# Performance work log

Hardware: AMD Instinct MI355X
Metric: run time of the kernel (lower is better)

Reference implementation:

```python
import jax, jax.numpy as jnp
import numpy as np

B, L, N = 16, 64, 1024
HAND_DIM, J, HID = 99, 21, 512
N_LAYERS, N_HEADS = 4, 8
DH = HID // N_HEADS
CAT = HAND_DIM + 2 * J * 3 + 2 * N  # 2273
PNAMES = ['fc_lw','fc_lb','fc_rw','fc_rb','out_lw','out_lb','out_rw','out_rb','Wqkv','bqkv','Wo','bo','W1','b1f','W2','b2f','ln1_g','ln1_b','ln2_g','ln2_b']

def sinusoidal_pe(n_pos, d):
    pos = np.arange(n_pos)[:, None].astype(np.float32)
    div = np.exp(np.arange(0, d, 2).astype(np.float32) * (-np.log(10000.0) / d))
    pe = np.zeros((n_pos, d), np.float32)
    pe[:, 0::2] = np.sin(pos * div)
    pe[:, 1::2] = np.cos(pos * div)
    return jnp.asarray(pe)

def rot6d_to_rotmat(x6):
    a1, a2 = x6[..., 0:3], x6[..., 3:6]
    b1 = a1 / jnp.linalg.norm(a1, axis=-1, keepdims=True)
    b2 = a2 - jnp.sum(b1 * a2, -1, keepdims=True) * b1
    b2 = b2 / jnp.linalg.norm(b2, axis=-1, keepdims=True)
    b3 = jnp.cross(b1, b2)
    return jnp.stack([b1, b2, b3], axis=-1)  # [..., 3, 3] (columns)

def layer_norm(x, g, b):
    mu = jnp.mean(x, -1, keepdims=True)
    var = jnp.mean((x - mu) ** 2, -1, keepdims=True)
    return (x - mu) * jax.lax.rsqrt(var + 1e-5) * g + b

def attention_map(joints, pc):
    # joints [B,L,J,3], pc [B,L,N,3]; squared dists via ||a||^2+||b||^2-2ab (no [B,L,J,N,3] diff tensor)
    d2 = (jnp.sum(joints ** 2, -1)[..., :, None] + jnp.sum(pc ** 2, -1)[..., None, :]
          - 2.0 * jnp.einsum('bljd,blnd->bljn', joints, pc))
    idx = jnp.argmin(d2, axis=-1)  # [B,L,J] nearest-point index
    idx3 = jnp.broadcast_to(idx[..., None], idx.shape + (3,))
    contact = jnp.take_along_axis(pc, idx3, axis=2)  # [B,L,J,3]
    return jnp.exp(-50.0 * (joints - contact) ** 2)

def mha(x, Wqkv, bqkv, Wo, bo):
    Bq, S, D = x.shape
    qkv = x @ Wqkv + bqkv
    q, k, v = jnp.split(qkv, 3, axis=-1)
    split = lambda t: t.reshape(Bq, S, N_HEADS, DH).transpose(0, 2, 1, 3)
    q, k, v = split(q), split(k), split(v)
    att = jax.nn.softmax(jnp.einsum('bhqd,bhkd->bhqk', q, k) * (1.0 / np.sqrt(DH)), axis=-1)
    o = jnp.einsum('bhqk,bhkd->bhqd', att, v).transpose(0, 2, 1, 3).reshape(Bq, S, D)
    return o @ Wo + bo

def forward(x_lhand, x_rhand, j_lhand, j_rhand, m_contact, x_obj, point_cloud, p):
    rotmat = rot6d_to_rotmat(x_obj[..., 3:9])  # [B,L,3,3]
    pc_t = jnp.einsum('btij,bkj->btki', rotmat, point_cloud) + x_obj[..., 0:3][:, :, None, :]
    att_l = attention_map(j_lhand, pc_t).reshape(B, L, -1)
    att_r = attention_map(j_rhand, pc_t).reshape(B, L, -1)
    mc = jnp.broadcast_to(m_contact.reshape(B, 1, N), (B, L, N))
    pcn = jnp.linalg.norm(pc_t, axis=-1)  # [B,L,N]
    xl = jnp.concatenate([x_lhand, j_lhand.reshape(B, L, -1), mc, pcn, att_l], -1)
    xr = jnp.concatenate([x_rhand, j_rhand.reshape(B, L, -1), mc, pcn, att_r], -1)
    xl = xl @ p['fc_lw'] + p['fc_lb']
    xr = xr @ p['fc_rw'] + p['fc_rb']
    x = jnp.stack([xl, xr], axis=2).reshape(B, 2 * L, HID)  # interleave agents per frame
    pe_frame = jnp.repeat(sinusoidal_pe(L, HID), 2, axis=0)  # frame-wise: pair shares position
    pe_agent = jnp.tile(sinusoidal_pe(2, HID), (L, 1))       # agent-wise: alternating 0/1
    x = x + pe_frame[None] + pe_agent[None]
    for i in range(N_LAYERS):
        h = layer_norm(x + mha(x, p['Wqkv'][i], p['bqkv'][i], p['Wo'][i], p['bo'][i]), p['ln1_g'][i], p['ln1_b'][i])
        ff = jax.nn.relu(h @ p['W1'][i] + p['b1f'][i]) @ p['W2'][i] + p['b2f'][i]
        x = layer_norm(h + ff, p['ln2_g'][i], p['ln2_b'][i])
    out_l = x[:, 0::2] @ p['out_lw'] + p['out_lb']
    out_r = x[:, 1::2] @ p['out_rw'] + p['out_rb']
    return out_l, out_r

def setup_inputs() -> dict:
    key = jax.random.key(0)
    ks = jax.random.split(key, 16)
    r = lambda i, shape, s=1.0: jax.random.normal(ks[i], shape, jnp.float32) * s
    return {
        'x_lhand': r(0, (B, L, HAND_DIM)),
        'x_rhand': r(1, (B, L, HAND_DIM)),
        'j_lhand': r(2, (B, L, J, 3)),
        'j_rhand': r(3, (B, L, J, 3)),
        'm_contact': jax.random.uniform(ks[4], (B, N, 1), jnp.float32),
        'x_obj': r(5, (B, L, 10)),
        'point_cloud': r(6, (B, N, 3)),
        'fc_lw': r(7, (CAT, HID), 0.02), 'fc_lb': jnp.zeros((HID,), jnp.float32),
        'fc_rw': r(8, (CAT, HID), 0.02), 'fc_rb': jnp.zeros((HID,), jnp.float32),
        'out_lw': r(9, (HID, HAND_DIM), 0.02), 'out_lb': jnp.zeros((HAND_DIM,), jnp.float32),
        'out_rw': r(10, (HID, HAND_DIM), 0.02), 'out_rb': jnp.zeros((HAND_DIM,), jnp.float32),
        'Wqkv': r(11, (N_LAYERS, HID, 3 * HID), 0.02), 'bqkv': jnp.zeros((N_LAYERS, 3 * HID), jnp.float32),
        'Wo': r(12, (N_LAYERS, HID, HID), 0.02), 'bo': jnp.zeros((N_LAYERS, HID), jnp.float32),
        'W1': r(13, (N_LAYERS, HID, 4 * HID), 0.02), 'b1f': jnp.zeros((N_LAYERS, 4 * HID), jnp.float32),
        'W2': r(14, (N_LAYERS, 4 * HID, HID), 0.02), 'b2f': jnp.zeros((N_LAYERS, HID), jnp.float32),
        'ln1_g': jnp.ones((N_LAYERS, HID), jnp.float32), 'ln1_b': jnp.zeros((N_LAYERS, HID), jnp.float32),
        'ln2_g': jnp.ones((N_LAYERS, HID), jnp.float32), 'ln2_b': jnp.zeros((N_LAYERS, HID), jnp.float32),
    }

def reference(x_lhand, x_rhand, j_lhand, j_rhand, m_contact, x_obj, point_cloud, fc_lw, fc_lb, fc_rw, fc_rb, out_lw, out_lb, out_rw, out_rb, Wqkv, bqkv, Wo, bo, W1, b1f, W2, b2f, ln1_g, ln1_b, ln2_g, ln2_b):
    p = dict(zip(PNAMES, (fc_lw, fc_lb, fc_rw, fc_rb, out_lw, out_lb, out_rw, out_rb, Wqkv, bqkv, Wo, bo, W1, b1f, W2, b2f, ln1_g, ln1_b, ln2_g, ln2_b)))
    return forward(x_lhand, x_rhand, j_lhand, j_rhand, m_contact, x_obj, point_cloud, p)
```

## Files before the change

kernel.cpp:

```cpp
#include <hip/hip_runtime.h>
#include <hip/hip_bf16.h>

typedef __hip_bfloat16 bf16;
typedef __attribute__((ext_vector_type(8))) short short8;
typedef __attribute__((ext_vector_type(4))) float floatx4;

#define B_    16
#define L_    64
#define N_    1024
#define HANDD 99
#define Jn    21
#define HID   512
#define NLAY  4
#define NHEAD 8
#define DHEAD 64
#define CATD  2273
#define CATP  2304
#define S_    128
#define T_    2048

#define F_X     16
#define F_QKV   1048592
#define F_TMP   6291472
#define F_H     7340048
#define WB_F    8388624
#define W_FCL   0
#define W_FCR   1179648
#define W_QKV   2359296
#define W_WO    5505024
#define W_W1    6553600
#define W_W2    10747904
#define U_CATL  14942208
#define U_CATR  17301504
#define U_XB    19660800
#define U_AOB   20709376
#define U_HB    21757952
#define W_OUT   22806528
#define U_FFB   U_CATL

static __device__ __forceinline__ float b2f(bf16 x) { return __bfloat162float(x); }
static __device__ __forceinline__ float ldin(const void* p, size_t i, int isf32) {
    return isf32 ? ((const float*)p)[i] : b2f(((const bf16*)p)[i]);
}
static __device__ __forceinline__ unsigned short f2bf(float f) {
    unsigned int u = __float_as_uint(f);
    unsigned int r = (u + 0x7fffu + ((u >> 16) & 1u)) >> 16;
    return (unsigned short)r;
}

__global__ __launch_bounds__(256) void detect_kernel(const void* mc, int* flag)
{
    __shared__ int sbad;
    int tid = threadIdx.x;
    if (tid == 0) sbad = 0;
    __syncthreads();
    int bad = 0;
    for (int i = tid; i < 16384; i += 256) {
        float v = b2f(((const bf16*)mc)[i]);
        if (!(v >= -0.02f && v <= 1.02f)) bad = 1;
    }
    if (bad) atomicOr(&sbad, 1);
    __syncthreads();
    if (tid == 0) flag[0] = sbad ? 1 : 0;
}

__global__ __launch_bounds__(256) void wtrans_kernel(
    const void* __restrict__ src, size_t src_layer, int K, int Nn, int NnBound,
    int Kpad, unsigned short* __restrict__ dst, size_t dst_layer,
    const int* __restrict__ dtf)
{
    int isf32 = dtf[0];
    __shared__ float tile[64][65];
    int lay = blockIdx.z;
    size_t soff = (size_t)lay * src_layer;
    size_t doff = (size_t)lay * dst_layer;
    int n0 = blockIdx.x * 64, k0 = blockIdx.y * 64;
    int a = threadIdx.x & 63, bq = threadIdx.x >> 6;
    for (int r = bq; r < 64; r += 4) {
        int k = k0 + r;
        int n = n0 + a;
        float v = (k < K && n < NnBound) ? ldin(src, soff + (size_t)k * Nn + n, isf32) : 0.f;
        tile[r][a] = v;
    }
    __syncthreads();
    for (int r = bq; r < 64; r += 4) {
        dst[doff + (size_t)(n0 + r) * Kpad + k0 + a] = f2bf(tile[a][r]);
    }
}

__global__ __launch_bounds__(256) void pctcat_kernel(
    const void* __restrict__ x_l, const void* __restrict__ j_l,
    const void* __restrict__ x_r, const void* __restrict__ j_r,
    const void* __restrict__ mc, const void* __restrict__ x_obj,
    const void* __restrict__ pc, unsigned short* __restrict__ cat_l,
    unsigned short* __restrict__ cat_r, const int* __restrict__ dtf)
{
    __shared__ float pcl[N_ * 3];
    __shared__ float pcnl[N_];
    int isf32 = dtf[0];
    int bl = blockIdx.x;
    int b  = bl >> 6;
    int tid = threadIdx.x;

    size_t xo = (size_t)bl * 10;
    float t0 = ldin(x_obj, xo+0, isf32), t1 = ldin(x_obj, xo+1, isf32), t2 = ldin(x_obj, xo+2, isf32);
    float a1x = ldin(x_obj, xo+3, isf32), a1y = ldin(x_obj, xo+4, isf32), a1z = ldin(x_obj, xo+5, isf32);
    float a2x = ldin(x_obj, xo+6, isf32), a2y = ldin(x_obj, xo+7, isf32), a2z = ldin(x_obj, xo+8, isf32);
    float n1 = sqrtf(a1x*a1x + a1y*a1y + a1z*a1z);
    float b1x = a1x / n1, b1y = a1y / n1, b1z = a1z / n1;
    float d = b1x*a2x + b1y*a2y + b1z*a2z;
    float c2x = a2x - d*b1x, c2y = a2y - d*b1y, c2z = a2z - d*b1z;
    float n2 = sqrtf(c2x*c2x + c2y*c2y + c2z*c2z);
    float b2x = c2x / n2, b2y = c2y / n2, b2z = c2z / n2;
    float b3x = b1y*b2z - b1z*b2y;
    float b3y = b1z*b2x - b1x*b2z;
    float b3z = b1x*b2y - b1y*b2x;

    size_t pcb = (size_t)b * N_ * 3;
    for (int n = tid; n < N_; n += 256) {
        float p0 = ldin(pc, pcb + n*3+0, isf32);
        float p1 = ldin(pc, pcb + n*3+1, isf32);
        float p2 = ldin(pc, pcb + n*3+2, isf32);
        float q0 = b1x*p0 + b2x*p1 + b3x*p2 + t0;
        float q1 = b1y*p0 + b2y*p1 + b3y*p2 + t1;
        float q2 = b1z*p0 + b2z*p1 + b3z*p2 + t2;
        pcl[n*3+0] = q0; pcl[n*3+1] = q1; pcl[n*3+2] = q2;
        pcnl[n] = sqrtf(q0*q0 + q1*q1 + q2*q2);
    }
    __syncthreads();

    #pragma unroll
    for (int hand = 0; hand < 2; hand++) {
        const void* xh = hand ? x_r : x_l;
        const void* jh = hand ? j_r : j_l;
        unsigned short* row = (hand ? cat_r : cat_l) + (size_t)bl * CATP;
        for (int c = tid; c < HANDD; c += 256)  row[c]        = f2bf(ldin(xh, (size_t)bl*HANDD + c, isf32));
        for (int c = tid; c < 63;    c += 256)  row[99 + c]   = f2bf(ldin(jh, (size_t)bl*63 + c, isf32));
        for (int c = tid; c < N_;    c += 256)  row[162 + c]  = f2bf(ldin(mc, (size_t)b*N_ + c, isf32));
        for (int c = tid; c < N_;    c += 256)  row[1186 + c] = f2bf(pcnl[c]);
        for (int c = CATD + tid; c < CATP; c += 256) row[c] = 0;
    }

    int wave = tid >> 6, lane = tid & 63;
    for (int t = wave; t < 2 * Jn; t += 4) {
        int hand = t / Jn, j = t - hand * Jn;
        const void* jh = hand ? j_r : j_l;
        unsigned short* row = (hand ? cat_r : cat_l) + (size_t)bl * CATP;
        float jx = ldin(jh, (size_t)bl*63 + j*3 + 0, isf32);
        float jy = ldin(jh, (size_t)bl*63 + j*3 + 1, isf32);
        float jz = ldin(jh, (size_t)bl*63 + j*3 + 2, isf32);
        float jj = jx*jx + jy*jy + jz*jz;
        float best = 3.4e38f; int bidx = 0x7fffffff;
        for (int n = lane; n < N_; n += 64) {
            float p0 = pcl[n*3+0], p1 = pcl[n*3+1], p2 = pcl[n*3+2];
            float d2 = jj + (p0*p0 + p1*p1 + p2*p2) - 2.f*(jx*p0 + jy*p1 + jz*p2);
            if (d2 < best) { best = d2; bidx = n; }
        }
        for (int off = 32; off; off >>= 1) {
            float ob = __shfl_down(best, off, 64);
            int   oi = __shfl_down(bidx, off, 64);
            if (ob < best || (ob == best && oi < bidx)) { best = ob; bidx = oi; }
        }
        bidx = __shfl(bidx, 0, 64);
        if (lane < 3) {
            float jc = (lane == 0) ? jx : ((lane == 1) ? jy : jz);
            float cc = pcl[bidx*3 + lane];
            float dd = jc - cc;
            row[2210 + j*3 + lane] = f2bf(expf(-50.f * dd * dd));
        }
    }
}

#define RSTR 68

__global__ __launch_bounds__(256) void gemm_ks(
    const unsigned short* __restrict__ Ab, const unsigned short* __restrict__ Ab2,
    int K,
    const unsigned short* __restrict__ Wt, size_t wtoff, size_t wtoff2, int halfgrid,
    int Nn,
    const void* __restrict__ bias, const void* __restrict__ bias2, size_t boff,
    const float* __restrict__ resid,
    float* __restrict__ Df, unsigned short* __restrict__ Db,
    int relu, int rowmap, int tilesN, const int* __restrict__ dtf)
{
    __shared__ float red[4][64 * RSTR];
    int blk = blockIdx.x;
    if (halfgrid && blk >= halfgrid) {
        blk -= halfgrid; Ab = Ab2; wtoff = wtoff2; bias = bias2; rowmap = 2;
    }
    int tid = threadIdx.x;
    int wave = tid >> 6, lane = tid & 63;
    int quad = lane >> 4, l16 = lane & 15;
    int tm = blk / tilesN, tn = blk - tm * tilesN;
    int row0 = tm << 6, col0 = tn << 6;
    int Ks = K >> 2;
    int ks0 = wave * Ks;

    const unsigned short* Ap = Ab + (size_t)(row0 + l16) * K + ks0 + quad * 8;
    const unsigned short* Bp = Wt + wtoff + (size_t)(col0 + l16) * K + ks0 + quad * 8;
    size_t astep = (size_t)16 * K;

    floatx4 acc[4][4];
    #pragma unroll
    for (int i = 0; i < 4; i++)
        #pragma unroll
        for (int j = 0; j < 4; j++)
            acc[i][j] = (floatx4){0.f, 0.f, 0.f, 0.f};

    for (int k = 0; k < Ks; k += 32) {
        short8 af[4], bf[4];
        #pragma unroll
        for (int i = 0; i < 4; i++) {
            af[i] = *(const short8*)(Ap + i * astep + k);
            bf[i] = *(const short8*)(Bp + i * astep + k);
        }
        #pragma unroll
        for (int mi = 0; mi < 4; mi++)
            #pragma unroll
            for (int ni = 0; ni < 4; ni++)
                acc[mi][ni] = __builtin_amdgcn_mfma_f32_16x16x32_bf16(
                    af[mi], bf[ni], acc[mi][ni], 0, 0, 0);
    }

    #pragma unroll
    for (int mi = 0; mi < 4; mi++)
        #pragma unroll
        for (int ni = 0; ni < 4; ni++)
            #pragma unroll
            for (int reg = 0; reg < 4; reg++) {
                int r = mi * 16 + quad * 4 + reg;
                int c = ni * 16 + l16;
                red[wave][r * RSTR + c] = acc[mi][ni][reg];
            }
    __syncthreads();

    int isf32 = dtf[0];
    int cc = tid & 63;
    int c = col0 + cc;
    float bv;
    if (rowmap == 3)
        bv = (c < HANDD) ? ldin(bias, c, isf32)
           : ((c < 2 * HANDD) ? ldin(bias2, c - HANDD, isf32) : 0.f);
    else
        bv = bias ? ldin(bias, boff + c, isf32) : 0.f;
    float pe_div = 0.f, pa = 0.f;
    if (rowmap == 1 || rowmap == 2) {
        int ci = c & ~1;
        pe_div = expf((float)ci * (-logf(10000.f) / (float)HID));
        int hand = rowmap - 1;
        pa = (c & 1) ? cosf((float)hand * pe_div) : sinf((float)hand * pe_div);
    }
    int rbase = tid >> 6;
    #pragma unroll
    for (int j = 0; j < 16; j++) {
        int rr = rbase + (j << 2);
        int idx = rr * RSTR + cc;
        float v = red[0][idx] + red[1][idx] + red[2][idx] + red[3][idx] + bv;
        int r = row0 + rr;
        if (resid) v += resid[(size_t)r * Nn + c];
        if (relu)  v = fmaxf(v, 0.f);
        if (rowmap == 3) {
            int hand = r & 1;
            int l = (r >> 1) & 63, bb = r >> 7;
            if (hand == 0 && c < HANDD) {
                size_t oi = ((size_t)bb * 64 + l) * HANDD + c;
                if (isf32) ((float*)Df)[oi] = v;
                else       ((bf16*)Df)[oi]  = __float2bfloat16(v);
            } else if (hand == 1 && c >= HANDD && c < 2 * HANDD) {
                size_t oi = (size_t)B_ * L_ * HANDD + ((size_t)bb * 64 + l) * HANDD + (c - HANDD);
                if (isf32) ((float*)Df)[oi] = v;
                else       ((bf16*)Df)[oi]  = __float2bfloat16(v);
            }
        } else {
            int orow = r;
            if (rowmap) {
                int bb = r >> 6, ll = r & 63;
                orow = bb * S_ + 2 * ll + (rowmap - 1);
                float pf = (c & 1) ? cosf((float)ll * pe_div) : sinf((float)ll * pe_div);
                v += pf + pa;
            }
            if (Df) Df[(size_t)orow * Nn + c] = v;
            if (Db) Db[(size_t)orow * Nn + c] = f2bf(v);
        }
    }
}

#define VSTR 136

__global__ __launch_bounds__(128) void attn_mfma(
    const unsigned short* __restrict__ qkvb, unsigned short* __restrict__ aob)
{
    __shared__ unsigned short Vt[64 * VSTR];
    __shared__ unsigned short Pb[64 * VSTR];
    int bh = blockIdx.x;
    int b = bh >> 3, h = bh & 7;
    int rowhalf = blockIdx.y;
    int tid = threadIdx.x;
    int w = tid >> 6, lane = tid & 63;
    int quad = lane >> 4, l16 = lane & 15;
    size_t qbase = (size_t)(b * S_) * 1536 + h * DHEAD;

    for (int i = tid; i < S_ * DHEAD; i += 128) {
        int key = i >> 6, dcol = i & 63;
        Vt[dcol * VSTR + key] = qkvb[qbase + (size_t)key * 1536 + 1024 + dcol];
    }
    __syncthreads();

    int qrow0 = rowhalf * 64 + w * 32;
    short8 aQ[2][2];
    #pragma unroll
    for (int mt = 0; mt < 2; mt++)
        #pragma unroll
        for (int kc = 0; kc < 2; kc++)
            aQ[mt][kc] = *(const short8*)&qkvb[qbase + (size_t)(qrow0 + mt*16 + l16) * 1536 + kc*32 + quad*8];

    floatx4 sacc[2][8];
    #pragma unroll
    for (int mt = 0; mt < 2; mt++)
        #pragma unroll
        for (int nt = 0; nt < 8; nt++)
            sacc[mt][nt] = (floatx4){0.f, 0.f, 0.f, 0.f};

    #pragma unroll
    for (int nt = 0; nt < 8; nt++) {
        const unsigned short* kp = &qkvb[qbase + (size_t)(nt*16 + l16) * 1536 + 512 + quad*8];
        short8 bK0 = *(const short8*)kp;
        short8 bK1 = *(const short8*)(kp + 32);
        #pragma unroll
        for (int mt = 0; mt < 2; mt++) {
            sacc[mt][nt] = __builtin_amdgcn_mfma_f32_16x16x32_bf16(aQ[mt][0], bK0, sacc[mt][nt], 0, 0, 0);
            sacc[mt][nt] = __builtin_amdgcn_mfma_f32_16x16x32_bf16(aQ[mt][1], bK1, sacc[mt][nt], 0, 0, 0);
        }
    }

    #pragma unroll
    for (int mt = 0; mt < 2; mt++)
        #pragma unroll
        for (int reg = 0; reg < 4; reg++) {
            float v[8];
            float m = -3.4e38f;
            #pragma unroll
            for (int nt = 0; nt < 8; nt++) { v[nt] = sacc[mt][nt][reg] * 0.125f; m = fmaxf(m, v[nt]); }
            #pragma unroll
            for (int off = 1; off <= 8; off <<= 1) m = fmaxf(m, __shfl_xor(m, off, 64));
            float sum = 0.f;
            #pragma unroll
            for (int nt = 0; nt < 8; nt++) { v[nt] = expf(v[nt] - m); sum += v[nt]; }
            #pragma unroll
            for (int off = 1; off <= 8; off <<= 1) sum += __shfl_xor(sum, off, 64);
            float inv = 1.f / sum;
            int lr = w*32 + mt*16 + quad*4 + reg;
            #pragma unroll
            for (int nt = 0; nt < 8; nt++)
                Pb[lr * VSTR + nt*16 + l16] = f2bf(v[nt] * inv);
        }
    __syncthreads();

    #pragma unroll
    for (int mt = 0; mt < 2; mt++) {
        short8 aP[4];
        #pragma unroll
        for (int kt = 0; kt < 4; kt++)
            aP[kt] = *(const short8*)&Pb[(w*32 + mt*16 + l16) * VSTR + kt*32 + quad*8];
        #pragma unroll
        for (int nt = 0; nt < 4; nt++) {
            floatx4 o = (floatx4){0.f, 0.f, 0.f, 0.f};
            #pragma unroll
            for (int kt = 0; kt < 4; kt++) {
                short8 bV = *(const short8*)&Vt[(nt*16 + l16) * VSTR + kt*32 + quad*8];
                o = __builtin_amdgcn_mfma_f32_16x16x32_bf16(aP[kt], bV, o, 0, 0, 0);
            }
            #pragma unroll
            for (int reg = 0; reg < 4; reg++) {
                int qrow = qrow0 + mt*16 + quad*4 + reg;
                aob[(size_t)(b*S_ + qrow) * HID + h*DHEAD + nt*16 + l16] = f2bf(o[reg]);
            }
        }
    }
}

__global__ __launch_bounds__(256) void ln_kernel(
    const float* __restrict__ src, const void* __restrict__ g,
    const void* __restrict__ bb, size_t goff,
    float* __restrict__ dst, unsigned short* __restrict__ dstb,
    const int* __restrict__ dtf)
{
    int isf32 = dtf[0];
    int t = blockIdx.x;
    const float* x = src + (size_t)t * HID;
    int tid = threadIdx.x, lane = tid & 63, wave = tid >> 6;
    float v0 = x[tid], v1 = x[tid + 256];
    float s = v0 + v1;
    for (int off = 32; off; off >>= 1) s += __shfl_down(s, off, 64);
    __shared__ float wsum[4];
    if (lane == 0) wsum[wave] = s;
    __syncthreads();
    float mu = (wsum[0] + wsum[1] + wsum[2] + wsum[3]) * (1.f / 512.f);
    float d0 = v0 - mu, d1 = v1 - mu;
    float q = d0 * d0 + d1 * d1;
    for (int off = 32; off; off >>= 1) q += __shfl_down(q, off, 64);
    __syncthreads();
    if (lane == 0) wsum[wave] = q;
    __syncthreads();
    float var = (wsum[0] + wsum[1] + wsum[2] + wsum[3]) * (1.f / 512.f);
    float rstd = 1.f / sqrtf(var + 1e-5f);
    float y0 = d0 * rstd * ldin(g, goff + tid, isf32)       + ldin(bb, goff + tid, isf32);
    float y1 = d1 * rstd * ldin(g, goff + tid + 256, isf32) + ldin(bb, goff + tid + 256, isf32);
    if (dst) {
        dst[(size_t)t * HID + tid]       = y0;
        dst[(size_t)t * HID + tid + 256] = y1;
    }
    if (dstb) {
        dstb[(size_t)t * HID + tid]       = f2bf(y0);
        dstb[(size_t)t * HID + tid + 256] = f2bf(y1);
    }
}

extern "C" void kernel_launch(void* const* d_in, const int* in_sizes, int n_in,
                              void* d_out, int out_size, void* d_ws, size_t ws_size,
                              hipStream_t stream)
{
    const void* x_lhand = d_in[0];
    const void* x_rhand = d_in[1];
    const void* j_lhand = d_in[2];
    const void* j_rhand = d_in[3];
    const void* m_contact = d_in[4];
    const void* x_obj = d_in[5];
    const void* point_cloud = d_in[6];
    const void* fc_lw = d_in[7];
    const void* fc_lb = d_in[8];
    const void* fc_rw = d_in[9];
    const void* fc_rb = d_in[10];
    const void* out_lw = d_in[11];
    const void* out_lb = d_in[12];
    const void* out_rw = d_in[13];
    const void* out_rb = d_in[14];
    const void* Wqkv = d_in[15];
    const void* bqkv = d_in[16];
    const void* Wo   = d_in[17];
    const void* bo   = d_in[18];
    const void* W1   = d_in[19];
    const void* b1f  = d_in[20];
    const void* W2   = d_in[21];
    const void* b2fp = d_in[22];
    const void* ln1g = d_in[23];
    const void* ln1b = d_in[24];
    const void* ln2g = d_in[25];
    const void* ln2b = d_in[26];

    float* ws = (float*)d_ws;
    int* dtf = (int*)d_ws;
    float* x     = ws + F_X;
    float* tmp   = ws + F_TMP;
    float* h     = ws + F_H;
    unsigned short* qkvb = (unsigned short*)(ws + F_QKV);
    unsigned short* wb   = (unsigned short*)(ws + WB_F);
    unsigned short* catl = wb + U_CATL;
    unsigned short* catr = wb + U_CATR;
    unsigned short* xb   = wb + U_XB;
    unsigned short* aob  = wb + U_AOB;
    unsigned short* hb   = wb + U_HB;
    unsigned short* ffb  = wb + U_FFB;

    detect_kernel<<<1, 256, 0, stream>>>(m_contact, dtf);

    wtrans_kernel<<<dim3(8, 36, 1), 256, 0, stream>>>(fc_lw, 0, CATD, HID, HID, CATP, wb + W_FCL, 0, dtf);
    wtrans_kernel<<<dim3(8, 36, 1), 256, 0, stream>>>(fc_rw, 0, CATD, HID, HID, CATP, wb + W_FCR, 0, dtf);
    wtrans_kernel<<<dim3(24, 8, NLAY), 256, 0, stream>>>(Wqkv, (size_t)HID*1536, HID, 1536, 1536, HID, wb + W_QKV, (size_t)1536*HID, dtf);
    wtrans_kernel<<<dim3(8, 8, NLAY), 256, 0, stream>>>(Wo, (size_t)HID*HID, HID, HID, HID, HID, wb + W_WO, (size_t)HID*HID, dtf);
    wtrans_kernel<<<dim3(32, 8, NLAY), 256, 0, stream>>>(W1, (size_t)HID*2048, HID, 2048, 2048, HID, wb + W_W1, (size_t)2048*HID, dtf);
    wtrans_kernel<<<dim3(8, 32, NLAY), 256, 0, stream>>>(W2, (size_t)2048*HID, 2048, HID, HID, 2048, wb + W_W2, (size_t)HID*2048, dtf);
    wtrans_kernel<<<dim3(2, 8, 1), 256, 0, stream>>>(out_lw, 0, HID, HANDD, HANDD, HID, wb + W_OUT, 0, dtf);
    wtrans_kernel<<<dim3(2, 8, 1), 256, 0, stream>>>(out_rw, 0, HID, HANDD, HANDD, HID, wb + W_OUT + (size_t)HANDD * HID, 0, dtf);

    pctcat_kernel<<<B_ * L_, 256, 0, stream>>>(
        x_lhand, j_lhand, x_rhand, j_rhand, m_contact, x_obj, point_cloud,
        catl, catr, dtf);

    gemm_ks<<<256, 256, 0, stream>>>(catl, catr, CATP, wb, W_FCL, W_FCR, 128, HID,
                                     fc_lb, fc_rb, 0, nullptr, x, xb, 0, 1, 8, dtf);

    for (int i = 0; i < NLAY; i++) {
        size_t oWq = (size_t)W_QKV + (size_t)i * 1536 * HID, obq = (size_t)i * 1536;
        size_t oWo = (size_t)W_WO + (size_t)i * HID * HID,   obo = (size_t)i * HID;
        size_t oW1 = (size_t)W_W1 + (size_t)i * 2048 * HID,  ob1 = (size_t)i * 2048;
        size_t oW2 = (size_t)W_W2 + (size_t)i * HID * 2048,  ob2 = (size_t)i * HID;
        size_t oln = (size_t)i * HID;

        gemm_ks<<<768, 256, 0, stream>>>(xb, nullptr, HID, wb, oWq, 0, 0, 1536,
                                         bqkv, nullptr, obq, nullptr, nullptr, qkvb, 0, 0, 24, dtf);

        attn_mfma<<<dim3(B_ * NHEAD, 2), 128, 0, stream>>>(qkvb, aob);

        gemm_ks<<<256, 256, 0, stream>>>(aob, nullptr, HID, wb, oWo, 0, 0, HID,
                                         bo, nullptr, obo, x, tmp, nullptr, 0, 0, 8, dtf);
        ln_kernel<<<T_, 256, 0, stream>>>(tmp, ln1g, ln1b, oln, h, hb, dtf);

        gemm_ks<<<1024, 256, 0, stream>>>(hb, nullptr, HID, wb, oW1, 0, 0, 2048,
                                          b1f, nullptr, ob1, nullptr, nullptr, ffb, 1, 0, 32, dtf);
        gemm_ks<<<256, 256, 0, stream>>>(ffb, nullptr, 2048, wb, oW2, 0, 0, HID,
                                         b2fp, nullptr, ob2, h, tmp, nullptr, 0, 0, 8, dtf);
        ln_kernel<<<T_, 256, 0, stream>>>(tmp, ln2g, ln2b, oln, x, xb, dtf);
    }

    gemm_ks<<<128, 256, 0, stream>>>(xb, nullptr, HID, wb, W_OUT, 0, 0, 256,
                                     out_lb, out_rb, 0, nullptr, (float*)d_out, nullptr, 0, 3, 4, dtf);
}
```

Measured before the change: 721.6 us.

## Fuse weight transposes, cache point norms, and split gemm into row and K halves

Merges the eight weight-transpose launches into one block-indexed kernel to cut launch overhead. Precomputes per-point squared norms in shared memory and drops the constant joint term from the nearest-point search. Reworks the split-K gemm from four K slices to a 2x2 row-half by K-half layout, reducing the shared-memory reduction buffer fourfold and fusing the final sum with register accumulators. This trades longer per-wave K loops for higher occupancy and less reduction traffic.

```diff
diff --git a/kernel.cpp b/kernel.cpp
--- a/kernel.cpp
+++ b/kernel.cpp
@@ -64,27 +64,61 @@
     if (tid == 0) flag[0] = sbad ? 1 : 0;
 }
 
-__global__ __launch_bounds__(256) void wtrans_kernel(
-    const void* __restrict__ src, size_t src_layer, int K, int Nn, int NnBound,
-    int Kpad, unsigned short* __restrict__ dst, size_t dst_layer,
-    const int* __restrict__ dtf)
-{
+__global__ __launch_bounds__(256) void wtrans_all(
+    const void* __restrict__ fc_lw, const void* __restrict__ fc_rw,
+    const void* __restrict__ Wqkv, const void* __restrict__ Wo,
+    const void* __restrict__ W1, const void* __restrict__ W2,
+    const void* __restrict__ out_lw, const void* __restrict__ out_rw,
+    unsigned short* __restrict__ wb, const int* __restrict__ dtf)
+{
+    int blk = blockIdx.x;
+    const void* src; unsigned short* dst;
+    size_t slay, dlay; int K, Nn, NnB, Kpad, nx, ny, rem, wclip = 1 << 30;
+    if (blk < 576) {
+        int half = blk >= 288; rem = blk - (half ? 288 : 0);
+        src = half ? fc_rw : fc_lw; dst = wb + (half ? W_FCR : W_FCL);
+        nx = 8; ny = 36; slay = 0; dlay = 0; K = CATD; Nn = HID; NnB = HID; Kpad = CATP;
+    } else if (blk < 1344) {
+        rem = blk - 576; src = Wqkv; dst = wb + W_QKV;
+        nx = 24; ny = 8; slay = (size_t)HID * 1536; dlay = (size_t)1536 * HID;
+        K = HID; Nn = 1536; NnB = 1536; Kpad = HID;
+    } else if (blk < 1600) {
+        rem = blk - 1344; src = Wo; dst = wb + W_WO;
+        nx = 8; ny = 8; slay = (size_t)HID * HID; dlay = (size_t)HID * HID;
+        K = HID; Nn = HID; NnB = HID; Kpad = HID;
+    } else if (blk < 2624) {
+        rem = blk - 1600; src = W1; dst = wb + W_W1;
+        nx = 32; ny = 8; slay = (size_t)HID * 2048; dlay = (size_t)2048 * HID;
+        K = HID; Nn = 2048; NnB = 2048; Kpad = HID;
+    } else if (blk < 3648) {
+        rem = blk - 2624; src = W2; dst = wb + W_W2;
+        nx = 8; ny = 32; slay = (size_t)2048 * HID; dlay = (size_t)HID * 2048;
+        K = 2048; Nn = HID; NnB = HID; Kpad = 2048;
+    } else {
+        int half = blk >= 3664; rem = blk - (half ? 3664 : 3648);
+        src = half ? out_rw : out_lw;
+        dst = wb + W_OUT + (half ? (size_t)HANDD * HID : 0);
+        nx = 2; ny = 8; slay = 0; dlay = 0; K = HID; Nn = HANDD; NnB = HANDD; Kpad = HID;
+        if (!half) wclip = HANDD;
+    }
+    int bx = rem % nx; int t2 = rem / nx; int by = t2 % ny; int lay = t2 / ny;
+
     int isf32 = dtf[0];
     __shared__ float tile[64][65];
-    int lay = blockIdx.z;
-    size_t soff = (size_t)lay * src_layer;
-    size_t doff = (size_t)lay * dst_layer;
-    int n0 = blockIdx.x * 64, k0 = blockIdx.y * 64;
+    size_t soff = (size_t)lay * slay;
+    size_t doff = (size_t)lay * dlay;
+    int n0 = bx * 64, k0 = by * 64;
     int a = threadIdx.x & 63, bq = threadIdx.x >> 6;
     for (int r = bq; r < 64; r += 4) {
         int k = k0 + r;
         int n = n0 + a;
-        float v = (k < K && n < NnBound) ? ldin(src, soff + (size_t)k * Nn + n, isf32) : 0.f;
+        float v = (k < K && n < NnB) ? ldin(src, soff + (size_t)k * Nn + n, isf32) : 0.f;
         tile[r][a] = v;
     }
     __syncthreads();
     for (int r = bq; r < 64; r += 4) {
-        dst[doff + (size_t)(n0 + r) * Kpad + k0 + a] = f2bf(tile[a][r]);
+        if (n0 + r < wclip)
+            dst[doff + (size_t)(n0 + r) * Kpad + k0 + a] = f2bf(tile[a][r]);
     }
 }
 
@@ -97,6 +131,7 @@
 {
     __shared__ float pcl[N_ * 3];
     __shared__ float pcnl[N_];
+    __shared__ float pp[N_];
     int isf32 = dtf[0];
     int bl = blockIdx.x;
     int b  = bl >> 6;
@@ -125,7 +160,9 @@
         float q1 = b1y*p0 + b2y*p1 + b3y*p2 + t1;
         float q2 = b1z*p0 + b2z*p1 + b3z*p2 + t2;
         pcl[n*3+0] = q0; pcl[n*3+1] = q1; pcl[n*3+2] = q2;
-        pcnl[n] = sqrtf(q0*q0 + q1*q1 + q2*q2);
+        float s2 = q0*q0 + q1*q1 + q2*q2;
+        pp[n] = s2;
+        pcnl[n] = sqrtf(s2);
     }
     __syncthreads();
 
@@ -149,11 +186,10 @@
         float jx = ldin(jh, (size_t)bl*63 + j*3 + 0, isf32);
         float jy = ldin(jh, (size_t)bl*63 + j*3 + 1, isf32);
         float jz = ldin(jh, (size_t)bl*63 + j*3 + 2, isf32);
-        float jj = jx*jx + jy*jy + jz*jz;
         float best = 3.4e38f; int bidx = 0x7fffffff;
         for (int n = lane; n < N_; n += 64) {
-            float p0 = pcl[n*3+0], p1 = pcl[n*3+1], p2 = pcl[n*3+2];
-            float d2 = jj + (p0*p0 + p1*p1 + p2*p2) - 2.f*(jx*p0 + jy*p1 + jz*p2);
+            float dot = jx*pcl[n*3+0] + jy*pcl[n*3+1] + jz*pcl[n*3+2];
+            float d2 = pp[n] - 2.f * dot;
             if (d2 < best) { best = d2; bidx = n; }
         }
         for (int off = 32; off; off >>= 1) {
@@ -183,104 +219,108 @@
     float* __restrict__ Df, unsigned short* __restrict__ Db,
     int relu, int rowmap, int tilesN, const int* __restrict__ dtf)
 {
-    __shared__ float red[4][64 * RSTR];
+    __shared__ float red[2][32 * RSTR];
     int blk = blockIdx.x;
     if (halfgrid && blk >= halfgrid) {
         blk -= halfgrid; Ab = Ab2; wtoff = wtoff2; bias = bias2; rowmap = 2;
     }
     int tid = threadIdx.x;
-    int wave = tid >> 6, lane = tid & 63;
+    int w = tid >> 6, lane = tid & 63;
+    int rh = w >> 1, kh = w & 1;
     int quad = lane >> 4, l16 = lane & 15;
     int tm = blk / tilesN, tn = blk - tm * tilesN;
     int row0 = tm << 6, col0 = tn << 6;
-    int Ks = K >> 2;
-    int ks0 = wave * Ks;
-
-    const unsigned short* Ap = Ab + (size_t)(row0 + l16) * K + ks0 + quad * 8;
+    int Ks = K >> 1;
+    int ks0 = kh * Ks;
+
+    const unsigned short* Ap = Ab + (size_t)(row0 + rh * 32 + l16) * K + ks0 + quad * 8;
     const unsigned short* Bp = Wt + wtoff + (size_t)(col0 + l16) * K + ks0 + quad * 8;
     size_t astep = (size_t)16 * K;
 
-    floatx4 acc[4][4];
-    #pragma unroll
-    for (int i = 0; i < 4; i++)
+    floatx4 acc[2][4];
+    #pragma unroll
+    for (int i = 0; i < 2; i++)
         #pragma unroll
         for (int j = 0; j < 4; j++)
             acc[i][j] = (floatx4){0.f, 0.f, 0.f, 0.f};
 
     for (int k = 0; k < Ks; k += 32) {
-        short8 af[4], bf[4];
-        #pragma unroll
-        for (int i = 0; i < 4; i++) {
-            af[i] = *(const short8*)(Ap + i * astep + k);
+        short8 af[2], bf[4];
+        af[0] = *(const short8*)(Ap + k);
+        af[1] = *(const short8*)(Ap + astep + k);
+        #pragma unroll
+        for (int i = 0; i < 4; i++)
             bf[i] = *(const short8*)(Bp + i * astep + k);
-        }
-        #pragma unroll
-        for (int mi = 0; mi < 4; mi++)
+        #pragma unroll
+        for (int mi = 0; mi < 2; mi++)
             #pragma unroll
             for (int ni = 0; ni < 4; ni++)
                 acc[mi][ni] = __builtin_amdgcn_mfma_f32_16x16x32_bf16(
                     af[mi], bf[ni], acc[mi][ni], 0, 0, 0);
     }
 
-    #pragma unroll
-    for (int mi = 0; mi < 4; mi++)
-        #pragma unroll
-        for (int ni = 0; ni < 4; ni++)
-            #pragma unroll
-            for (int reg = 0; reg < 4; reg++) {
-                int r = mi * 16 + quad * 4 + reg;
-                int c = ni * 16 + l16;
-                red[wave][r * RSTR + c] = acc[mi][ni][reg];
+    if (kh) {
+        #pragma unroll
+        for (int mi = 0; mi < 2; mi++)
+            #pragma unroll
+            for (int ni = 0; ni < 4; ni++)
+                #pragma unroll
+                for (int reg = 0; reg < 4; reg++)
+                    red[rh][(mi*16 + quad*4 + reg) * RSTR + ni*16 + l16] = acc[mi][ni][reg];
+    }
+    __syncthreads();
+    if (!kh) {
+        int isf32 = dtf[0];
+        #pragma unroll
+        for (int ni = 0; ni < 4; ni++) {
+            int c = col0 + ni*16 + l16;
+            float bv;
+            if (rowmap == 3)
+                bv = (c < HANDD) ? ldin(bias, c, isf32)
+                   : ((c < 2 * HANDD) ? ldin(bias2, c - HANDD, isf32) : 0.f);
+            else
+                bv = bias ? ldin(bias, boff + c, isf32) : 0.f;
+            float pe_div = 0.f, pa = 0.f;
+            if (rowmap == 1 || rowmap == 2) {
+                int ci = c & ~1;
+                pe_div = expf((float)ci * (-logf(10000.f) / (float)HID));
+                int hand = rowmap - 1;
+                pa = (c & 1) ? cosf((float)hand * pe_div) : sinf((float)hand * pe_div);
             }
-    __syncthreads();
-
-    int isf32 = dtf[0];
-    int cc = tid & 63;
-    int c = col0 + cc;
-    float bv;
-    if (rowmap == 3)
-        bv = (c < HANDD) ? ldin(bias, c, isf32)
-           : ((c < 2 * HANDD) ? ldin(bias2, c - HANDD, isf32) : 0.f);
-    else
-        bv = bias ? ldin(bias, boff + c, isf32) : 0.f;
-    float pe_div = 0.f, pa = 0.f;
-    if (rowmap == 1 || rowmap == 2) {
-        int ci = c & ~1;
-        pe_div = expf((float)ci * (-logf(10000.f) / (float)HID));
-        int hand = rowmap - 1;
-        pa = (c & 1) ? cosf((float)hand * pe_div) : sinf((float)hand * pe_div);
-    }
-    int rbase = tid >> 6;
-    #pragma unroll
-    for (int j = 0; j < 16; j++) {
-        int rr = rbase + (j << 2);
-        int idx = rr * RSTR + cc;
-        float v = red[0][idx] + red[1][idx] + red[2][idx] + red[3][idx] + bv;
-        int r = row0 + rr;
-        if (resid) v += resid[(size_t)r * Nn + c];
-        if (relu)  v = fmaxf(v, 0.f);
-        if (rowmap == 3) {
-            int hand = r & 1;
-            int l = (r >> 1) & 63, bb = r >> 7;
-            if (hand == 0 && c < HANDD) {
-                size_t oi = ((size_t)bb * 64 + l) * HANDD + c;
-                if (isf32) ((float*)Df)[oi] = v;
-                else       ((bf16*)Df)[oi]  = __float2bfloat16(v);
-            } else if (hand == 1 && c >= HANDD && c < 2 * HANDD) {
-                size_t oi = (size_t)B_ * L_ * HANDD + ((size_t)bb * 64 + l) * HANDD + (c - HANDD);
-                if (isf32) ((float*)Df)[oi] = v;
-                else       ((bf16*)Df)[oi]  = __float2bfloat16(v);
+            #pragma unroll
+            for (int mi = 0; mi < 2; mi++) {
+                #pragma unroll
+                for (int reg = 0; reg < 4; reg++) {
+                    int rl = mi*16 + quad*4 + reg;
+                    int r = row0 + rh*32 + rl;
+                    float v = acc[mi][ni][reg] + red[rh][rl * RSTR + ni*16 + l16] + bv;
+                    if (resid) v += resid[(size_t)r * Nn + c];
+                    if (relu)  v = fmaxf(v, 0.f);
+                    if (rowmap == 3) {
+                        int hand = r & 1;
+                        int l = (r >> 1) & 63, bb = r >> 7;
+                        if (hand == 0 && c < HANDD) {
+                            size_t oi = ((size_t)bb * 64 + l) * HANDD + c;
+                            if (isf32) ((float*)Df)[oi] = v;
+                            else       ((bf16*)Df)[oi]  = __float2bfloat16(v);
+                        } else if (hand == 1 && c >= HANDD && c < 2 * HANDD) {
+                            size_t oi = (size_t)B_ * L_ * HANDD + ((size_t)bb * 64 + l) * HANDD + (c - HANDD);
+                            if (isf32) ((float*)Df)[oi] = v;
+                            else       ((bf16*)Df)[oi]  = __float2bfloat16(v);
+                        }
+                    } else {
+                        int orow = r;
+                        if (rowmap) {
+                            int bb = r >> 6, ll = r & 63;
+                            orow = bb * S_ + 2 * ll + (rowmap - 1);
+                            float pf = (c & 1) ? cosf((float)ll * pe_div) : sinf((float)ll * pe_div);
+                            v += pf + pa;
+                        }
+                        if (Df) Df[(size_t)orow * Nn + c] = v;
+                        if (Db) Db[(size_t)orow * Nn + c] = f2bf(v);
+                    }
+                }
             }
-        } else {
-            int orow = r;
-            if (rowmap) {
-                int bb = r >> 6, ll = r & 63;
-                orow = bb * S_ + 2 * ll + (rowmap - 1);
-                float pf = (c & 1) ? cosf((float)ll * pe_div) : sinf((float)ll * pe_div);
-                v += pf + pa;
-            }
-            if (Df) Df[(size_t)orow * Nn + c] = v;
-            if (Db) Db[(size_t)orow * Nn + c] = f2bf(v);
         }
     }
 }
@@ -464,14 +504,8 @@
 
     detect_kernel<<<1, 256, 0, stream>>>(m_contact, dtf);
 
-    wtrans_kernel<<<dim3(8, 36, 1), 256, 0, stream>>>(fc_lw, 0, CATD, HID, HID, CATP, wb + W_FCL, 0, dtf);
-    wtrans_kernel<<<dim3(8, 36, 1), 256, 0, stream>>>(fc_rw, 0, CATD, HID, HID, CATP, wb + W_FCR, 0, dtf);
-    wtrans_kernel<<<dim3(24, 8, NLAY), 256, 0, stream>>>(Wqkv, (size_t)HID*1536, HID, 1536, 1536, HID, wb + W_QKV, (size_t)1536*HID, dtf);
-    wtrans_kernel<<<dim3(8, 8, NLAY), 256, 0, stream>>>(Wo, (size_t)HID*HID, HID, HID, HID, HID, wb + W_WO, (size_t)HID*HID, dtf);
-    wtrans_kernel<<<dim3(32, 8, NLAY), 256, 0, stream>>>(W1, (size_t)HID*2048, HID, 2048, 2048, HID, wb + W_W1, (size_t)2048*HID, dtf);
-    wtrans_kernel<<<dim3(8, 32, NLAY), 256, 0, stream>>>(W2, (size_t)2048*HID, 2048, HID, HID, 2048, wb + W_W2, (size_t)HID*2048, dtf);
-    wtrans_kernel<<<dim3(2, 8, 1), 256, 0, stream>>>(out_lw, 0, HID, HANDD, HANDD, HID, wb + W_OUT, 0, dtf);
-    wtrans_kernel<<<dim3(2, 8, 1), 256, 0, stream>>>(out_rw, 0, HID, HANDD, HANDD, HID, wb + W_OUT + (size_t)HANDD * HID, 0, dtf);
+    wtrans_all<<<3680, 256, 0, stream>>>(fc_lw, fc_rw, Wqkv, Wo, W1, W2,
+                                         out_lw, out_rw, wb, dtf);
 
     pctcat_kernel<<<B_ * L_, 256, 0, stream>>>(
         x_lhand, j_lhand, x_rhand, j_rhand, m_contact, x_obj, point_cloud,
```

Result: slower. 845.0 us (+17.1%).
